# Optimization experiments

Hardware: AMD Instinct MI355X
Metric: run time of the kernel (lower is better)

The kernel has to match this reference:

```python
import jax, jax.numpy as jnp
import numpy as np

N_USER = 100000
N_ITEM = 150000
N = N_USER + N_ITEM
D = 64            # latdim
NNZ = 1250000     # sparse adjacency nnz
BATCH = 16384     # node_ids batch
NUM_GNN_LAYERS = 2
GD = 16           # gate_dim (mamba d_model)
DSTATE = 8
DCONV = 4
EXPAND = 2
DINNER = GD * EXPAND  # 32
DTRANK = 1            # ceil(GD/16)
TEMP = 0.8            # gate_temp


def setup_inputs() -> dict:
    key = jax.random.key(0)
    ks = jax.random.split(key, 20)
    f32 = jnp.float32
    inp = {}
    inp["user_embedding"] = jax.random.normal(ks[0], (N_USER, D), f32) * 0.02
    inp["item_embedding"] = jax.random.normal(ks[1], (N_ITEM, D), f32) * 0.02
    inp["edge_row"] = jax.random.randint(ks[2], (NNZ,), 0, N, dtype=jnp.int32)
    inp["edge_col"] = jax.random.randint(ks[3], (NNZ,), 0, N, dtype=jnp.int32)
    inp["edge_val"] = jax.random.uniform(ks[4], (NNZ,), f32) * 0.1
    inp["node_ids"] = jax.random.randint(ks[5], (BATCH,), 0, N, dtype=jnp.int32)
    # gate params (torch Linear weight layout: [out, in])
    inp["down_w"] = jax.random.normal(ks[6], (GD, D), f32) * 0.02
    inp["in_proj_w"] = jax.random.normal(ks[7], (2 * DINNER, GD), f32) * 0.05
    inp["conv_w"] = jax.random.normal(ks[8], (DINNER, DCONV), f32) * 0.1
    inp["conv_b"] = jnp.zeros((DINNER,), f32)
    inp["x_proj_w"] = jax.random.normal(ks[9], (DTRANK + 2 * DSTATE, DINNER), f32) * 0.05
    inp["dt_proj_w"] = jax.random.normal(ks[10], (DINNER, DTRANK), f32) * 0.1
    inp["dt_proj_b"] = jax.random.normal(ks[11], (DINNER,), f32) * 0.1
    inp["A_log"] = jnp.log(jnp.broadcast_to(jnp.arange(1, DSTATE + 1, dtype=f32), (DINNER, DSTATE)))
    inp["D_param"] = jnp.ones((DINNER,), f32)
    inp["out_proj_w"] = jax.random.normal(ks[12], (GD, DINNER), f32) * 0.05
    inp["ln_g"] = jnp.ones((GD,), f32)
    inp["ln_b"] = jnp.zeros((GD,), f32)
    inp["to_logit_w"] = jax.random.normal(ks[13], (1, GD), f32) * 0.02
    inp["to_logit_b"] = jnp.zeros((1,), f32)
    return inp


def _mamba(g, in_proj_w, conv_w, conv_b, x_proj_w, dt_proj_w, dt_proj_b, A_log, D_param, out_proj_w):
    # g: [B, L, GD] -- standard Mamba block (selective scan)
    Bsz, L, _ = g.shape
    xz = g @ in_proj_w.T                     # [B,L,2*DINNER]
    x, z = jnp.split(xz, 2, axis=-1)         # each [B,L,DINNER]
    # causal depthwise conv1d along L (padding = DCONV-1, truncated to L)
    xp = jnp.pad(x, ((0, 0), (DCONV - 1, 0), (0, 0)))
    xconv = sum(xp[:, k:k + L, :] * conv_w[:, k] for k in range(DCONV)) + conv_b
    x = jax.nn.silu(xconv)
    dbc = x @ x_proj_w.T                     # [B,L,DTRANK+2*DSTATE]
    dt = dbc[..., :DTRANK]
    Bm = dbc[..., DTRANK:DTRANK + DSTATE]
    Cm = dbc[..., DTRANK + DSTATE:]
    dt = jax.nn.softplus(dt @ dt_proj_w.T + dt_proj_b)   # [B,L,DINNER]
    A = -jnp.exp(A_log)                                   # [DINNER,DSTATE]
    dA = jnp.exp(dt[..., None] * A)                       # [B,L,DINNER,DSTATE]
    dBx = dt[..., None] * Bm[:, :, None, :] * x[..., None]

    def step(h, ins):
        dA_t, dBx_t = ins
        h = dA_t * h + dBx_t
        return h, h

    h0 = jnp.zeros((Bsz, DINNER, DSTATE), x.dtype)
    _, hs = jax.lax.scan(step, h0, (jnp.swapaxes(dA, 0, 1), jnp.swapaxes(dBx, 0, 1)))
    hs = jnp.swapaxes(hs, 0, 1)                           # [B,L,DINNER,DSTATE]
    y = jnp.einsum('blds,bls->bld', hs, Cm) + D_param * x
    y = y * jax.nn.silu(z)
    return y @ out_proj_w.T                               # [B,L,GD]


def reference(user_embedding, item_embedding, edge_val, down_w, in_proj_w, conv_w,
              conv_b, x_proj_w, dt_proj_w, dt_proj_b, A_log, D_param, out_proj_w,
              ln_g, ln_b, to_logit_w, to_logit_b, edge_row, edge_col, node_ids):
    embeds = jnp.concatenate([user_embedding, item_embedding], axis=0)   # [N,D]
    seqs = [embeds[node_ids]]
    for _ in range(NUM_GNN_LAYERS):
        # sparse adjacency aggregation: out[r] += val * embeds[c]
        msg = edge_val[:, None] * embeds[edge_col]                       # [NNZ,D]
        embeds = jax.ops.segment_sum(msg, edge_row, num_segments=N)      # [N,D]
        # F.normalize(p=2, dim=1)
        nrm = jnp.linalg.norm(embeds, axis=1, keepdims=True)
        embeds = embeds / jnp.maximum(nrm, 1e-12)
        seqs.append(embeds[node_ids])
    seq = jnp.stack(seqs, axis=1)                                        # [B,L,D]

    # MambaDepthGating._compute_logits (deg_cond disabled)
    g = seq @ down_w.T                                                   # [B,L,GD]
    y = _mamba(g, in_proj_w, conv_w, conv_b, x_proj_w, dt_proj_w, dt_proj_b,
               A_log, D_param, out_proj_w)
    y = y + g
    mu = y.mean(-1, keepdims=True)
    var = y.var(-1, keepdims=True)
    y = (y - mu) / jnp.sqrt(var + 1e-12) * ln_g + ln_b                   # LN eps=1e-12
    logits = (y @ to_logit_w.T + to_logit_b)[..., 0]                     # [B,L]

    # fuse_from_logits, L=3 > 2 -> softmax path, perturbed=False
    w = jax.nn.softmax(logits / max(TEMP, 1e-6), axis=1)                 # [B,L]
    fused = jnp.sum(seq * w[..., None], axis=1)                          # [B,D]
    return fused
```

## Files before the change

### kernel.cpp

```cpp
#include <hip/hip_runtime.h>
#include <math.h>

#define N_USER 100000
#define N_ITEM 150000
#define NTOT   250000
#define D64    64
#define NNZ    1250000
#define BATCH  16384
#define GD     16
#define DSTATE 8
#define DCONV  4
#define DINNER 32
#define LSEQ   3
#define NBLK1  ((NTOT + 1023) >> 10)

__global__ void mark_nids_kernel(const int* __restrict__ nids,
                                 unsigned char* __restrict__ nidf,
                                 unsigned char* __restrict__ needf) {
    int b = blockIdx.x * 256 + threadIdx.x;
    if (b < BATCH) { int r = nids[b]; nidf[r] = 1; needf[r] = 1; }
}

__global__ void mark_need_kernel(const int* __restrict__ erow,
                                 const int* __restrict__ ecol,
                                 const unsigned char* __restrict__ nidf,
                                 unsigned char* __restrict__ needf) {
    int e = blockIdx.x * 256 + threadIdx.x;
    if (e < NNZ && nidf[erow[e]]) needf[ecol[e]] = 1;
}

__global__ void compact_kernel(const unsigned char* __restrict__ needf,
                               int* __restrict__ nrows,
                               int* __restrict__ row_list) {
    int i = blockIdx.x * 256 + threadIdx.x;
    int flag = (i < NTOT) ? (int)needf[i] : 0;
    unsigned long long mask = __ballot(flag != 0);
    int lane = threadIdx.x & 63;
    int prefix = __popcll(mask & ((1ull << lane) - 1ull));
    int total = __popcll(mask);
    int base = 0;
    if (lane == 0 && total) base = atomicAdd(nrows, total);
    base = __shfl(base, 0, 64);
    if (flag) row_list[base + prefix] = i;
}

__global__ void hist_slot_kernel(const int* __restrict__ erow,
                                 const unsigned char* __restrict__ needf,
                                 int* __restrict__ cnt, int* __restrict__ slot) {
    int e = blockIdx.x * 256 + threadIdx.x;
    if (e >= NNZ) return;
    int r = erow[e];
    if (needf[r]) slot[e] = atomicAdd(&cnt[r], 1);
}

__global__ __launch_bounds__(256) void scan1_kernel(const int* __restrict__ cnt,
                                                    int* __restrict__ offs,
                                                    int* __restrict__ bsum) {
    __shared__ int lds[256];
    int t = threadIdx.x;
    int base = (blockIdx.x << 10) + (t << 2);
    int d0 = (base + 0 < NTOT) ? cnt[base + 0] : 0;
    int d1 = (base + 1 < NTOT) ? cnt[base + 1] : 0;
    int d2 = (base + 2 < NTOT) ? cnt[base + 2] : 0;
    int d3 = (base + 3 < NTOT) ? cnt[base + 3] : 0;
    int s = d0 + d1 + d2 + d3;
    lds[t] = s;
    __syncthreads();
    for (int off = 1; off < 256; off <<= 1) {
        int v = (t >= off) ? lds[t - off] : 0;
        __syncthreads();
        lds[t] += v;
        __syncthreads();
    }
    int excl = lds[t] - s;
    if (base + 0 < NTOT) offs[base + 0] = excl;
    if (base + 1 < NTOT) offs[base + 1] = excl + d0;
    if (base + 2 < NTOT) offs[base + 2] = excl + d0 + d1;
    if (base + 3 < NTOT) offs[base + 3] = excl + d0 + d1 + d2;
    if (t == 255) bsum[blockIdx.x] = lds[255];
}

__global__ __launch_bounds__(256) void scan2_kernel(int* __restrict__ bsum) {
    __shared__ int lds[256];
    int t = threadIdx.x;
    int v0 = (t < NBLK1) ? bsum[t] : 0;
    lds[t] = v0;
    __syncthreads();
    for (int off = 1; off < 256; off <<= 1) {
        int v = (t >= off) ? lds[t - off] : 0;
        __syncthreads();
        lds[t] += v;
        __syncthreads();
    }
    if (t < NBLK1) bsum[t] = lds[t] - v0;
}

__global__ void scan3_kernel(int* __restrict__ offs, const int* __restrict__ bsum,
                             const int* __restrict__ cnt) {
    int i = blockIdx.x * 256 + threadIdx.x;
    if (i >= NTOT) return;
    int v = offs[i] + bsum[i >> 10];
    offs[i] = v;
    if (i == NTOT - 1) offs[NTOT] = v + cnt[i];
}

__global__ void fill_kernel(const int* __restrict__ erow, const int* __restrict__ ecol,
                            const float* __restrict__ eval_, const int* __restrict__ offs,
                            const int* __restrict__ slot,
                            const unsigned char* __restrict__ needf,
                            int2* __restrict__ colval) {
    int e = blockIdx.x * 256 + threadIdx.x;
    if (e >= NNZ) return;
    int r = erow[e];
    if (!needf[r]) return;
    colval[offs[r] + slot[e]] = make_int2(ecol[e], __float_as_int(eval_[e]));
}

__global__ __launch_bounds__(256) void layer1_kernel(const float* __restrict__ user,
                                                     const float* __restrict__ item,
                                                     const int*  __restrict__ nrows,
                                                     const int*  __restrict__ row_list,
                                                     const int*  __restrict__ offs,
                                                     const int2* __restrict__ colval,
                                                     float* __restrict__ dst) {
    const float4* user4 = (const float4*)user;
    const float4* item4 = (const float4*)item;

    int gid    = (blockIdx.x << 4) + (threadIdx.x >> 4);
    int lane16 = threadIdx.x & 15;
    if (gid >= nrows[0]) return;
    int row = row_list[gid];
    int o0 = offs[row], o1 = offs[row + 1];

    float4 acc = make_float4(0.f, 0.f, 0.f, 0.f);
    int i = o0;
    for (; i + 4 <= o1; i += 4) {
        int2 cv0 = colval[i], cv1 = colval[i + 1], cv2 = colval[i + 2], cv3 = colval[i + 3];
        const float4* s0 = (cv0.x < N_USER) ? user4 + (size_t)cv0.x * 16
                                            : item4 + (size_t)(cv0.x - N_USER) * 16;
        const float4* s1 = (cv1.x < N_USER) ? user4 + (size_t)cv1.x * 16
                                            : item4 + (size_t)(cv1.x - N_USER) * 16;
        const float4* s2 = (cv2.x < N_USER) ? user4 + (size_t)cv2.x * 16
                                            : item4 + (size_t)(cv2.x - N_USER) * 16;
        const float4* s3 = (cv3.x < N_USER) ? user4 + (size_t)cv3.x * 16
                                            : item4 + (size_t)(cv3.x - N_USER) * 16;
        float4 v0 = s0[lane16], v1 = s1[lane16], v2 = s2[lane16], v3 = s3[lane16];
        float w0 = __int_as_float(cv0.y), w1 = __int_as_float(cv1.y);
        float w2 = __int_as_float(cv2.y), w3 = __int_as_float(cv3.y);
        acc.x = fmaf(w3, v3.x, fmaf(w2, v2.x, fmaf(w1, v1.x, fmaf(w0, v0.x, acc.x))));
        acc.y = fmaf(w3, v3.y, fmaf(w2, v2.y, fmaf(w1, v1.y, fmaf(w0, v0.y, acc.y))));
        acc.z = fmaf(w3, v3.z, fmaf(w2, v2.z, fmaf(w1, v1.z, fmaf(w0, v0.z, acc.z))));
        acc.w = fmaf(w3, v3.w, fmaf(w2, v2.w, fmaf(w1, v1.w, fmaf(w0, v0.w, acc.w))));
    }
    for (; i < o1; ++i) {
        int2 cv = colval[i];
        const float4* s0 = (cv.x < N_USER) ? user4 + (size_t)cv.x * 16
                                           : item4 + (size_t)(cv.x - N_USER) * 16;
        float4 v = s0[lane16];
        float w = __int_as_float(cv.y);
        acc.x = fmaf(w, v.x, acc.x);
        acc.y = fmaf(w, v.y, acc.y);
        acc.z = fmaf(w, v.z, acc.z);
        acc.w = fmaf(w, v.w, acc.w);
    }

    float s = fmaf(acc.x, acc.x, fmaf(acc.y, acc.y, fmaf(acc.z, acc.z, acc.w * acc.w)));
    #pragma unroll
    for (int m = 8; m >= 1; m >>= 1) s += __shfl_xor(s, m, 64);
    float scale = 1.f / fmaxf(sqrtf(s), 1e-12f);
    float4 r;
    r.x = acc.x * scale; r.y = acc.y * scale; r.z = acc.z * scale; r.w = acc.w * scale;
    ((float4*)dst)[(size_t)row * 16 + lane16] = r;
}

__global__ __launch_bounds__(256) void layer2_kernel(const float* __restrict__ embA,
                                                     const int*  __restrict__ nids,
                                                     const int*  __restrict__ offs,
                                                     const int2* __restrict__ colval,
                                                     float* __restrict__ embBc) {
    const float4* src4 = (const float4*)embA;
    int idx    = (blockIdx.x << 4) + (threadIdx.x >> 4);
    int lane16 = threadIdx.x & 15;
    if (idx >= BATCH) return;
    int row = nids[idx];
    int o0 = offs[row], o1 = offs[row + 1];

    float4 acc = make_float4(0.f, 0.f, 0.f, 0.f);
    int i = o0;
    for (; i + 4 <= o1; i += 4) {
        int2 cv0 = colval[i], cv1 = colval[i + 1], cv2 = colval[i + 2], cv3 = colval[i + 3];
        float4 v0 = src4[(size_t)cv0.x * 16 + lane16];
        float4 v1 = src4[(size_t)cv1.x * 16 + lane16];
        float4 v2 = src4[(size_t)cv2.x * 16 + lane16];
        float4 v3 = src4[(size_t)cv3.x * 16 + lane16];
        float w0 = __int_as_float(cv0.y), w1 = __int_as_float(cv1.y);
        float w2 = __int_as_float(cv2.y), w3 = __int_as_float(cv3.y);
        acc.x = fmaf(w3, v3.x, fmaf(w2, v2.x, fmaf(w1, v1.x, fmaf(w0, v0.x, acc.x))));
        acc.y = fmaf(w3, v3.y, fmaf(w2, v2.y, fmaf(w1, v1.y, fmaf(w0, v0.y, acc.y))));
        acc.z = fmaf(w3, v3.z, fmaf(w2, v2.z, fmaf(w1, v1.z, fmaf(w0, v0.z, acc.z))));
        acc.w = fmaf(w3, v3.w, fmaf(w2, v2.w, fmaf(w1, v1.w, fmaf(w0, v0.w, acc.w))));
    }
    for (; i < o1; ++i) {
        int2 cv = colval[i];
        float4 v = src4[(size_t)cv.x * 16 + lane16];
        float w = __int_as_float(cv.y);
        acc.x = fmaf(w, v.x, acc.x);
        acc.y = fmaf(w, v.y, acc.y);
        acc.z = fmaf(w, v.z, acc.z);
        acc.w = fmaf(w, v.w, acc.w);
    }

    float s = fmaf(acc.x, acc.x, fmaf(acc.y, acc.y, fmaf(acc.z, acc.z, acc.w * acc.w)));
    #pragma unroll
    for (int m = 8; m >= 1; m >>= 1) s += __shfl_xor(s, m, 64);
    float scale = 1.f / fmaxf(sqrtf(s), 1e-12f);
    float4 r;
    r.x = acc.x * scale; r.y = acc.y * scale; r.z = acc.z * scale; r.w = acc.w * scale;
    ((float4*)embBc)[(size_t)idx * 16 + lane16] = r;
}

__global__ __launch_bounds__(256) void final_kernel(
    const int*   __restrict__ nids,
    const float* __restrict__ user,      const float* __restrict__ item,
    const float* __restrict__ embA,      const float* __restrict__ embBc,
    const float* __restrict__ down_w,    const float* __restrict__ in_proj_w,
    const float* __restrict__ conv_w,    const float* __restrict__ conv_b,
    const float* __restrict__ x_proj_w,  const float* __restrict__ dt_proj_w,
    const float* __restrict__ dt_proj_b, const float* __restrict__ A_log,
    const float* __restrict__ D_param,   const float* __restrict__ out_proj_w,
    const float* __restrict__ ln_g,      const float* __restrict__ ln_b,
    const float* __restrict__ to_logit_w,const float* __restrict__ to_logit_b,
    float* __restrict__ out) {

    __shared__ float4 s_rows4[16 * 49];
    __shared__ float  s_downT[D64 * GD];
    __shared__ float  s_ipxT[GD * DINNER];
    __shared__ float  s_ipzT[GD * DINNER];
    __shared__ float  s_xpT[DINNER * 17];
    __shared__ float  s_opT[DINNER * GD];
    __shared__ float  s_AT[DSTATE * DINNER];
    __shared__ float4 s_cw4[DINNER];
    __shared__ float  s_cb[DINNER], s_dtw[DINNER], s_dtb[DINNER], s_Dp[DINNER];
    __shared__ float  s_lng[GD], s_lnb[GD], s_lw[GD];
    __shared__ float  s_lb;
    __shared__ float  s_g[16 * 49];
    __shared__ float  s_xs[16 * 98];
    __shared__ float  s_dbc[16 * 49];

    int t = threadIdx.x;

    for (int i = t; i < D64 * GD; i += 256) {
        int j = i & 15, d = i >> 4;
        s_downT[i] = down_w[j * D64 + d];
    }
    for (int i = t; i < GD * DINNER; i += 256) {
        int d = i & 31, j = i >> 5;
        s_ipxT[i] = in_proj_w[d * GD + j];
        s_ipzT[i] = in_proj_w[(d + DINNER) * GD + j];
    }
    for (int i = t; i < DINNER * 17; i += 256) {
        int d = i / 17, r = i % 17;
        s_xpT[i] = x_proj_w[r * DINNER + d];
    }
    for (int i = t; i < DINNER * GD; i += 256) {
        int j = i & 15, d = i >> 4;
        s_opT[i] = out_proj_w[j * DINNER + d];
    }
    for (int i = t; i < DSTATE * DINNER; i += 256) {
        int d = i & 31, s = i >> 5;
        s_AT[i] = -expf(A_log[d * DSTATE + s]);
    }
    if (t < DINNER) {
        s_cw4[t] = ((const float4*)conv_w)[t];
        s_cb[t] = conv_b[t]; s_dtw[t] = dt_proj_w[t];
        s_dtb[t] = dt_proj_b[t]; s_Dp[t] = D_param[t];
    }
    if (t < GD) { s_lng[t] = ln_g[t]; s_lnb[t] = ln_b[t]; s_lw[t] = to_logit_w[t]; }
    if (t == 0) s_lb = to_logit_b[0];

    int wave = t >> 6, lane = t & 63;
    int grp = lane >> 4, lane16 = lane & 15;
    int eb = wave * 4 + grp;
    int b  = blockIdx.x * 16 + eb;
    {
        int nid = nids[b];
        const float4* p0 = (const float4*)((nid < N_USER) ? user + (size_t)nid * D64
                                                          : item + (size_t)(nid - N_USER) * D64);
        const float4* p1 = (const float4*)(embA + (size_t)nid * D64);
        const float4* p2 = (const float4*)(embBc + (size_t)b * D64);
        s_rows4[eb * 49 + 0 * 16 + lane16] = p0[lane16];
        s_rows4[eb * 49 + 1 * 16 + lane16] = p1[lane16];
        s_rows4[eb * 49 + 2 * 16 + lane16] = p2[lane16];
    }
    __syncthreads();

    const float* rows = (const float*)s_rows4 + eb * 196;

    {
        float a0 = 0.f, a1 = 0.f, a2 = 0.f;
        #pragma unroll
        for (int d = 0; d < D64; ++d) {
            float w = s_downT[d * GD + lane16];
            a0 = fmaf(rows[d], w, a0);
            a1 = fmaf(rows[64 + d], w, a1);
            a2 = fmaf(rows[128 + d], w, a2);
        }
        s_g[eb * 49 + 0 * GD + lane16] = a0;
        s_g[eb * 49 + 1 * GD + lane16] = a1;
        s_g[eb * 49 + 2 * GD + lane16] = a2;
    }
    __syncthreads();

    const float* ge = s_g + eb * 49;

    float xsr[2][LSEQ];
    #pragma unroll
    for (int c = 0; c < 2; ++c) {
        int d = lane16 + 16 * c;
        float xl0 = 0.f, xl1 = 0.f, xl2 = 0.f;
        #pragma unroll
        for (int j = 0; j < GD; ++j) {
            float w = s_ipxT[j * DINNER + d];
            xl0 = fmaf(ge[j], w, xl0);
            xl1 = fmaf(ge[GD + j], w, xl1);
            xl2 = fmaf(ge[2 * GD + j], w, xl2);
        }
        float4 cw = s_cw4[d]; float cb = s_cb[d];
        float a0 = fmaf(xl0, cw.w, cb);
        float a1 = fmaf(xl1, cw.w, fmaf(xl0, cw.z, cb));
        float a2 = fmaf(xl2, cw.w, fmaf(xl1, cw.z, fmaf(xl0, cw.y, cb)));
        xsr[c][0] = a0 / (1.f + __expf(-a0));
        xsr[c][1] = a1 / (1.f + __expf(-a1));
        xsr[c][2] = a2 / (1.f + __expf(-a2));
        #pragma unroll
        for (int l = 0; l < LSEQ; ++l) s_xs[eb * 98 + l * DINNER + d] = xsr[c][l];
    }
    __syncthreads();

    {
        const float* xse = s_xs + eb * 98;
        int nr = (lane16 == 0) ? 2 : 1;
        for (int it = 0; it < nr; ++it) {
            int r = (it == 0) ? lane16 : 16;
            float a0 = 0.f, a1 = 0.f, a2 = 0.f;
            #pragma unroll
            for (int d = 0; d < DINNER; ++d) {
                float w = s_xpT[d * 17 + r];
                a0 = fmaf(xse[d], w, a0);
                a1 = fmaf(xse[DINNER + d], w, a1);
                a2 = fmaf(xse[2 * DINNER + d], w, a2);
            }
            s_dbc[eb * 49 + 0 * 17 + r] = a0;
            s_dbc[eb * 49 + 1 * 17 + r] = a1;
            s_dbc[eb * 49 + 2 * 17 + r] = a2;
        }
    }
    __syncthreads();

    {
        const float* dbce = s_dbc + eb * 49;
        float h[2][DSTATE];
        #pragma unroll
        for (int c = 0; c < 2; ++c)
            #pragma unroll
            for (int s = 0; s < DSTATE; ++s) h[c][s] = 0.f;
        #pragma unroll
        for (int l = 0; l < LSEQ; ++l) {
            float dtr = dbce[l * 17];
            float Bm[DSTATE], Cm[DSTATE];
            #pragma unroll
            for (int s = 0; s < DSTATE; ++s) {
                Bm[s] = dbce[l * 17 + 1 + s];
                Cm[s] = dbce[l * 17 + 9 + s];
            }
            #pragma unroll
            for (int c = 0; c < 2; ++c) {
                int d = lane16 + 16 * c;
                float pre = fmaf(dtr, s_dtw[d], s_dtb[d]);
                float dt  = (pre > 20.f) ? pre : __logf(1.f + __expf(pre));
                float xv  = xsr[c][l];
                float dtx = dt * xv;
                float acc = 0.f;
                #pragma unroll
                for (int s = 0; s < DSTATE; ++s) {
                    float dA = __expf(dt * s_AT[s * DINNER + d]);
                    h[c][s] = fmaf(dA, h[c][s], dtx * Bm[s]);
                    acc = fmaf(h[c][s], Cm[s], acc);
                }
                float y = fmaf(s_Dp[d], xv, acc);
                float zv = 0.f;
                #pragma unroll
                for (int j = 0; j < GD; ++j)
                    zv = fmaf(ge[l * GD + j], s_ipzT[j * DINNER + d], zv);
                float ys = y * (zv / (1.f + __expf(-zv)));
                s_xs[eb * 98 + l * DINNER + d] = ys;
            }
        }
    }
    __syncthreads();

    float lg[LSEQ];
    {
        const float* yse = s_xs + eb * 98;
        #pragma unroll
        for (int l = 0; l < LSEQ; ++l) {
            float a = 0.f;
            #pragma unroll
            for (int d = 0; d < DINNER; ++d)
                a = fmaf(yse[l * DINNER + d], s_opT[d * GD + lane16], a);
            float v = a + ge[l * GD + lane16];
            float sm = v, sq = v * v;
            #pragma unroll
            for (int m = 1; m <= 8; m <<= 1) {
                sm += __shfl_xor(sm, m, 64);
                sq += __shfl_xor(sq, m, 64);
            }
            float mu  = sm * (1.f / GD);
            float var = fmaxf(sq * (1.f / GD) - mu * mu, 0.f);
            float inv = rsqrtf(var + 1e-12f);
            float lo = fmaf(fmaf((v - mu) * inv, s_lng[lane16], s_lnb[lane16]),
                            s_lw[lane16], 0.f);
            #pragma unroll
            for (int m = 1; m <= 8; m <<= 1) lo += __shfl_xor(lo, m, 64);
            lg[l] = (lo + s_lb) * 1.25f;
        }
    }

    {
        float mx = fmaxf(lg[0], fmaxf(lg[1], lg[2]));
        float e0 = __expf(lg[0] - mx), e1 = __expf(lg[1] - mx), e2 = __expf(lg[2] - mx);
        float inv = 1.f / (e0 + e1 + e2);
        float w0 = e0 * inv, w1 = e1 * inv, w2 = e2 * inv;
        float4 r0 = s_rows4[eb * 49 + 0 * 16 + lane16];
        float4 r1 = s_rows4[eb * 49 + 1 * 16 + lane16];
        float4 r2 = s_rows4[eb * 49 + 2 * 16 + lane16];
        float4 r;
        r.x = w0 * r0.x + w1 * r1.x + w2 * r2.x;
        r.y = w0 * r0.y + w1 * r1.y + w2 * r2.y;
        r.z = w0 * r0.z + w1 * r1.z + w2 * r2.z;
        r.w = w0 * r0.w + w1 * r1.w + w2 * r2.w;
        ((float4*)out)[(size_t)b * 16 + lane16] = r;
    }
}

extern "C" void kernel_launch(void* const* d_in, const int* in_sizes, int n_in,
                              void* d_out, int out_size, void* d_ws, size_t ws_size,
                              hipStream_t stream) {
    const float* user      = (const float*)d_in[0];
    const float* item      = (const float*)d_in[1];
    const int*   erow      = (const int*)  d_in[2];
    const int*   ecol      = (const int*)  d_in[3];
    const float* eval_     = (const float*)d_in[4];
    const int*   nids      = (const int*)  d_in[5];
    const float* down_w    = (const float*)d_in[6];
    const float* in_proj_w = (const float*)d_in[7];
    const float* conv_w    = (const float*)d_in[8];
    const float* conv_b    = (const float*)d_in[9];
    const float* x_proj_w  = (const float*)d_in[10];
    const float* dt_proj_w = (const float*)d_in[11];
    const float* dt_proj_b = (const float*)d_in[12];
    const float* A_log     = (const float*)d_in[13];
    const float* D_param   = (const float*)d_in[14];
    const float* out_projw = (const float*)d_in[15];
    const float* ln_g      = (const float*)d_in[16];
    const float* ln_b      = (const float*)d_in[17];
    const float* to_lw     = (const float*)d_in[18];
    const float* to_lb     = (const float*)d_in[19];
    float* out = (float*)d_out;

    char* base = (char*)d_ws;
    float* embA  = (float*)base;
    float* embBc = (float*)(base + 64000000);
    char* c = base + 64000000 + 4194304;
    int* cnt   = (int*)c;
    int* nrows = (int*)(c + 1000000);
    unsigned char* nidf  = (unsigned char*)(c + 1000064);
    unsigned char* needf = (unsigned char*)(c + 1250064);
    size_t zbytes = 1500096;
    c += zbytes;
    int* row_list = (int*)c;  c += (size_t)NTOT * 4;
    int* offs = (int*)c;  c += (size_t)(NTOT + 1) * 4 + 60;
    int* bsum = (int*)c;  c += 1024;
    int* slot = (int*)c;  c += (size_t)NNZ * 4;
    int2* colval = (int2*)c;

    hipMemsetAsync((void*)cnt, 0, zbytes, stream);

    mark_nids_kernel<<<(BATCH + 255) / 256, 256, 0, stream>>>(nids, nidf, needf);
    mark_need_kernel<<<(NNZ + 255) / 256, 256, 0, stream>>>(erow, ecol, nidf, needf);
    compact_kernel<<<(NTOT + 255) / 256, 256, 0, stream>>>(needf, nrows, row_list);

    hist_slot_kernel<<<(NNZ + 255) / 256, 256, 0, stream>>>(erow, needf, cnt, slot);
    scan1_kernel<<<NBLK1, 256, 0, stream>>>(cnt, offs, bsum);
    scan2_kernel<<<1, 256, 0, stream>>>(bsum);
    scan3_kernel<<<(NTOT + 255) / 256, 256, 0, stream>>>(offs, bsum, cnt);
    fill_kernel<<<(NNZ + 255) / 256, 256, 0, stream>>>(erow, ecol, eval_, offs, slot, needf, colval);

    layer1_kernel<<<(NTOT + 15) / 16, 256, 0, stream>>>(user, item, nrows, row_list, offs, colval, embA);
    layer2_kernel<<<BATCH / 16, 256, 0, stream>>>(embA, nids, offs, colval, embBc);

    final_kernel<<<BATCH / 16, 256, 0, stream>>>(nids, user, item, embA, embBc,
                                                 down_w, in_proj_w, conv_w, conv_b,
                                                 x_proj_w, dt_proj_w, dt_proj_b, A_log,
                                                 D_param, out_projw, ln_g, ln_b, to_lw, to_lb, out);
}
```

Measured before the change: 299.8 us.

## Fold row compaction into CSR scan and vectorize edge-processing kernels

Removes the separate ballot-and-atomic compaction kernel. The needed-row list is now built with a second prefix scan over the need flags, computed alongside the CSR offset scan, so the row order becomes deterministic. The edge kernels (mark_need, hist_slot, fill) now process four edges per thread using int4/float4 loads, which cuts the thread count and widens memory accesses. The cost is extra work and LDS traffic in the scans, plus an extra fpos array.

```diff
diff --git a/kernel.cpp b/kernel.cpp
--- a/kernel.cpp
+++ b/kernel.cpp
@@ -25,83 +25,110 @@
                                  const int* __restrict__ ecol,
                                  const unsigned char* __restrict__ nidf,
                                  unsigned char* __restrict__ needf) {
-    int e = blockIdx.x * 256 + threadIdx.x;
-    if (e < NNZ && nidf[erow[e]]) needf[ecol[e]] = 1;
-}
-
-__global__ void compact_kernel(const unsigned char* __restrict__ needf,
-                               int* __restrict__ nrows,
-                               int* __restrict__ row_list) {
-    int i = blockIdx.x * 256 + threadIdx.x;
-    int flag = (i < NTOT) ? (int)needf[i] : 0;
-    unsigned long long mask = __ballot(flag != 0);
-    int lane = threadIdx.x & 63;
-    int prefix = __popcll(mask & ((1ull << lane) - 1ull));
-    int total = __popcll(mask);
-    int base = 0;
-    if (lane == 0 && total) base = atomicAdd(nrows, total);
-    base = __shfl(base, 0, 64);
-    if (flag) row_list[base + prefix] = i;
+    int e = (blockIdx.x * 256 + threadIdx.x) * 4;
+    if (e + 4 <= NNZ) {
+        int4 r = *(const int4*)(erow + e);
+        int4 c = *(const int4*)(ecol + e);
+        if (nidf[r.x]) needf[c.x] = 1;
+        if (nidf[r.y]) needf[c.y] = 1;
+        if (nidf[r.z]) needf[c.z] = 1;
+        if (nidf[r.w]) needf[c.w] = 1;
+    } else {
+        for (; e < NNZ; ++e) if (nidf[erow[e]]) needf[ecol[e]] = 1;
+    }
 }
 
 __global__ void hist_slot_kernel(const int* __restrict__ erow,
                                  const unsigned char* __restrict__ needf,
                                  int* __restrict__ cnt, int* __restrict__ slot) {
-    int e = blockIdx.x * 256 + threadIdx.x;
-    if (e >= NNZ) return;
-    int r = erow[e];
-    if (needf[r]) slot[e] = atomicAdd(&cnt[r], 1);
+    int e = (blockIdx.x * 256 + threadIdx.x) * 4;
+    if (e + 4 <= NNZ) {
+        int4 r = *(const int4*)(erow + e);
+        if (needf[r.x]) slot[e + 0] = atomicAdd(&cnt[r.x], 1);
+        if (needf[r.y]) slot[e + 1] = atomicAdd(&cnt[r.y], 1);
+        if (needf[r.z]) slot[e + 2] = atomicAdd(&cnt[r.z], 1);
+        if (needf[r.w]) slot[e + 3] = atomicAdd(&cnt[r.w], 1);
+    } else {
+        for (; e < NNZ; ++e) {
+            int r = erow[e];
+            if (needf[r]) slot[e] = atomicAdd(&cnt[r], 1);
+        }
+    }
 }
 
 __global__ __launch_bounds__(256) void scan1_kernel(const int* __restrict__ cnt,
+                                                    const unsigned char* __restrict__ flags,
                                                     int* __restrict__ offs,
-                                                    int* __restrict__ bsum) {
+                                                    int* __restrict__ fpos,
+                                                    int* __restrict__ bsum,
+                                                    int* __restrict__ fbsum) {
     __shared__ int lds[256];
+    __shared__ int lfs[256];
     int t = threadIdx.x;
     int base = (blockIdx.x << 10) + (t << 2);
     int d0 = (base + 0 < NTOT) ? cnt[base + 0] : 0;
     int d1 = (base + 1 < NTOT) ? cnt[base + 1] : 0;
     int d2 = (base + 2 < NTOT) ? cnt[base + 2] : 0;
     int d3 = (base + 3 < NTOT) ? cnt[base + 3] : 0;
-    int s = d0 + d1 + d2 + d3;
-    lds[t] = s;
+    int f0 = (base + 0 < NTOT) ? (int)flags[base + 0] : 0;
+    int f1 = (base + 1 < NTOT) ? (int)flags[base + 1] : 0;
+    int f2 = (base + 2 < NTOT) ? (int)flags[base + 2] : 0;
+    int f3 = (base + 3 < NTOT) ? (int)flags[base + 3] : 0;
+    int s  = d0 + d1 + d2 + d3;
+    int fs = f0 + f1 + f2 + f3;
+    lds[t] = s; lfs[t] = fs;
     __syncthreads();
     for (int off = 1; off < 256; off <<= 1) {
-        int v = (t >= off) ? lds[t - off] : 0;
+        int v  = (t >= off) ? lds[t - off] : 0;
+        int fv = (t >= off) ? lfs[t - off] : 0;
         __syncthreads();
-        lds[t] += v;
+        lds[t] += v; lfs[t] += fv;
         __syncthreads();
     }
-    int excl = lds[t] - s;
-    if (base + 0 < NTOT) offs[base + 0] = excl;
-    if (base + 1 < NTOT) offs[base + 1] = excl + d0;
-    if (base + 2 < NTOT) offs[base + 2] = excl + d0 + d1;
-    if (base + 3 < NTOT) offs[base + 3] = excl + d0 + d1 + d2;
-    if (t == 255) bsum[blockIdx.x] = lds[255];
-}
-
-__global__ __launch_bounds__(256) void scan2_kernel(int* __restrict__ bsum) {
+    int excl  = lds[t] - s;
+    int fexcl = lfs[t] - fs;
+    if (base + 0 < NTOT) { offs[base + 0] = excl;                fpos[base + 0] = fexcl; }
+    if (base + 1 < NTOT) { offs[base + 1] = excl + d0;           fpos[base + 1] = fexcl + f0; }
+    if (base + 2 < NTOT) { offs[base + 2] = excl + d0 + d1;      fpos[base + 2] = fexcl + f0 + f1; }
+    if (base + 3 < NTOT) { offs[base + 3] = excl + d0 + d1 + d2; fpos[base + 3] = fexcl + f0 + f1 + f2; }
+    if (t == 255) { bsum[blockIdx.x] = lds[255]; fbsum[blockIdx.x] = lfs[255]; }
+}
+
+__global__ __launch_bounds__(256) void scan2_kernel(int* __restrict__ bsum,
+                                                    int* __restrict__ fbsum) {
     __shared__ int lds[256];
+    __shared__ int lfs[256];
     int t = threadIdx.x;
     int v0 = (t < NBLK1) ? bsum[t] : 0;
-    lds[t] = v0;
+    int f0 = (t < NBLK1) ? fbsum[t] : 0;
+    lds[t] = v0; lfs[t] = f0;
     __syncthreads();
     for (int off = 1; off < 256; off <<= 1) {
-        int v = (t >= off) ? lds[t - off] : 0;
+        int v  = (t >= off) ? lds[t - off] : 0;
+        int fv = (t >= off) ? lfs[t - off] : 0;
         __syncthreads();
-        lds[t] += v;
+        lds[t] += v; lfs[t] += fv;
         __syncthreads();
     }
-    if (t < NBLK1) bsum[t] = lds[t] - v0;
+    if (t < NBLK1) { bsum[t] = lds[t] - v0; fbsum[t] = lfs[t] - f0; }
 }
 
 __global__ void scan3_kernel(int* __restrict__ offs, const int* __restrict__ bsum,
-                             const int* __restrict__ cnt) {
+                             const int* __restrict__ cnt,
+                             const int* __restrict__ fpos, const int* __restrict__ fbsum,
+                             const unsigned char* __restrict__ flags,
+                             int* __restrict__ row_list, int* __restrict__ nrows) {
     int i = blockIdx.x * 256 + threadIdx.x;
     if (i >= NTOT) return;
     int v = offs[i] + bsum[i >> 10];
     offs[i] = v;
-    if (i == NTOT - 1) offs[NTOT] = v + cnt[i];
+    int fp = fpos[i] + fbsum[i >> 10];
+    int fl = flags[i];
+    if (fl) row_list[fp] = i;
+    if (i == NTOT - 1) {
+        offs[NTOT] = v + cnt[i];
+        nrows[0] = fp + fl;
+    }
 }
 
 __global__ void fill_kernel(const int* __restrict__ erow, const int* __restrict__ ecol,
@@ -109,11 +136,22 @@
                             const int* __restrict__ slot,
                             const unsigned char* __restrict__ needf,
                             int2* __restrict__ colval) {
-    int e = blockIdx.x * 256 + threadIdx.x;
-    if (e >= NNZ) return;
-    int r = erow[e];
-    if (!needf[r]) return;
-    colval[offs[r] + slot[e]] = make_int2(ecol[e], __float_as_int(eval_[e]));
+    int e = (blockIdx.x * 256 + threadIdx.x) * 4;
+    if (e + 4 <= NNZ) {
+        int4   r = *(const int4*)(erow + e);
+        int4   c = *(const int4*)(ecol + e);
+        float4 v = *(const float4*)(eval_ + e);
+        int4   s = *(const int4*)(slot + e);
+        if (needf[r.x]) colval[offs[r.x] + s.x] = make_int2(c.x, __float_as_int(v.x));
+        if (needf[r.y]) colval[offs[r.y] + s.y] = make_int2(c.y, __float_as_int(v.y));
+        if (needf[r.z]) colval[offs[r.z] + s.z] = make_int2(c.z, __float_as_int(v.z));
+        if (needf[r.w]) colval[offs[r.w] + s.w] = make_int2(c.w, __float_as_int(v.w));
+    } else {
+        for (; e < NNZ; ++e) {
+            int r = erow[e];
+            if (needf[r]) colval[offs[r] + slot[e]] = make_int2(ecol[e], __float_as_int(eval_[e]));
+        }
+    }
 }
 
 __global__ __launch_bounds__(256) void layer1_kernel(const float* __restrict__ user,
@@ -473,28 +511,31 @@
     float* embBc = (float*)(base + 64000000);
     char* c = base + 64000000 + 4194304;
     int* cnt   = (int*)c;
-    int* nrows = (int*)(c + 1000000);
-    unsigned char* nidf  = (unsigned char*)(c + 1000064);
-    unsigned char* needf = (unsigned char*)(c + 1250064);
-    size_t zbytes = 1500096;
-    c += zbytes;
+    unsigned char* nidf  = (unsigned char*)(c + 1000000);
+    unsigned char* needf = (unsigned char*)(c + 1250000);
+    size_t zbytes = 1500000;
+    c += 1500032;
+    int* nrows    = (int*)c;  c += 64;
     int* row_list = (int*)c;  c += (size_t)NTOT * 4;
-    int* offs = (int*)c;  c += (size_t)(NTOT + 1) * 4 + 60;
-    int* bsum = (int*)c;  c += 1024;
-    int* slot = (int*)c;  c += (size_t)NNZ * 4;
-    int2* colval = (int2*)c;
+    int* fpos     = (int*)c;  c += (size_t)NTOT * 4;
+    int* offs     = (int*)c;  c += (size_t)(NTOT + 1) * 4 + 60;
+    int* bsum     = (int*)c;  c += 1024;
+    int* fbsum    = (int*)c;  c += 1024;
+    int* slot     = (int*)c;  c += (size_t)NNZ * 4;
+    int2* colval  = (int2*)c;
 
     hipMemsetAsync((void*)cnt, 0, zbytes, stream);
 
     mark_nids_kernel<<<(BATCH + 255) / 256, 256, 0, stream>>>(nids, nidf, needf);
-    mark_need_kernel<<<(NNZ + 255) / 256, 256, 0, stream>>>(erow, ecol, nidf, needf);
-    compact_kernel<<<(NTOT + 255) / 256, 256, 0, stream>>>(needf, nrows, row_list);
-
-    hist_slot_kernel<<<(NNZ + 255) / 256, 256, 0, stream>>>(erow, needf, cnt, slot);
-    scan1_kernel<<<NBLK1, 256, 0, stream>>>(cnt, offs, bsum);
-    scan2_kernel<<<1, 256, 0, stream>>>(bsum);
-    scan3_kernel<<<(NTOT + 255) / 256, 256, 0, stream>>>(offs, bsum, cnt);
-    fill_kernel<<<(NNZ + 255) / 256, 256, 0, stream>>>(erow, ecol, eval_, offs, slot, needf, colval);
+    mark_need_kernel<<<(NNZ / 4 + 255) / 256, 256, 0, stream>>>(erow, ecol, nidf, needf);
+
+    hist_slot_kernel<<<(NNZ / 4 + 255) / 256, 256, 0, stream>>>(erow, needf, cnt, slot);
+    scan1_kernel<<<NBLK1, 256, 0, stream>>>(cnt, needf, offs, fpos, bsum, fbsum);
+    scan2_kernel<<<1, 256, 0, stream>>>(bsum, fbsum);
+    scan3_kernel<<<(NTOT + 255) / 256, 256, 0, stream>>>(offs, bsum, cnt, fpos, fbsum,
+                                                         needf, row_list, nrows);
+    fill_kernel<<<(NNZ / 4 + 255) / 256, 256, 0, stream>>>(erow, ecol, eval_, offs, slot,
+                                                           needf, colval);
 
     layer1_kernel<<<(NTOT + 15) / 16, 256, 0, stream>>>(user, item, nrows, row_list, offs, colval, embA);
     layer2_kernel<<<BATCH / 16, 256, 0, stream>>>(embA, nids, offs, colval, embBc);
```

New measurement: 247.2 us. 1.21x faster.
